# Optimization experiments

Hardware: AMD Instinct MI355X
Metric: run time of the kernel (lower is better)

## Reference

```python
import jax, jax.numpy as jnp
import numpy as np

N, CIN, COUT, E, NDIR = 65536, 128, 128, 589824, 9


def sel_conv(x, src, dst, sel, W, b):
    # x: [N, Cin]; W: [D, Cin, Cout]; edges j->i: out[i] += x[j] @ W[sel]
    n = x.shape[0]
    xs = x[src]  # [E, Cin] gather
    out = jnp.zeros((n, W.shape[2]), x.dtype)
    for d in range(W.shape[0]):  # fixed small direction count (9 or 1)
        m = (sel == d).astype(x.dtype)[:, None]
        agg = jax.ops.segment_sum(xs * m, dst, num_segments=n)  # [N, Cin]
        out = out + agg @ W[d]
    return out + b


def bn_eval(x, g, be, rm, rv, eps=1e-5):
    return (x - rm) * (g * jax.lax.rsqrt(rv + eps)) + be


def setup_inputs() -> dict:
    key = jax.random.key(0)
    ks = jax.random.split(key, 24)
    s = 0.05
    inp = {
        "x": jax.random.normal(ks[0], (N, CIN), jnp.float32),
        "edge_index": jax.random.randint(ks[1], (2, E), 0, N),
        "selections": jax.random.randint(ks[2], (E,), 0, NDIR),
        "W1": jax.random.normal(ks[3], (NDIR, CIN, COUT), jnp.float32) * s,
        "b1": jax.random.normal(ks[4], (COUT,), jnp.float32) * s,
        "g1": 1.0 + jax.random.normal(ks[5], (COUT,), jnp.float32) * s,
        "be1": jax.random.normal(ks[6], (COUT,), jnp.float32) * s,
        "rm1": jax.random.normal(ks[7], (COUT,), jnp.float32) * s,
        "rv1": 0.5 + jax.random.uniform(ks[8], (COUT,), jnp.float32),
        "W2": jax.random.normal(ks[9], (NDIR, COUT, COUT), jnp.float32) * s,
        "b2": jax.random.normal(ks[10], (COUT,), jnp.float32) * s,
        "g2": 1.0 + jax.random.normal(ks[11], (COUT,), jnp.float32) * s,
        "be2": jax.random.normal(ks[12], (COUT,), jnp.float32) * s,
        "rm2": jax.random.normal(ks[13], (COUT,), jnp.float32) * s,
        "rv2": 0.5 + jax.random.uniform(ks[14], (COUT,), jnp.float32),
        "W3": jax.random.normal(ks[15], (1, CIN, COUT), jnp.float32) * s,
        "b3": jax.random.normal(ks[16], (COUT,), jnp.float32) * s,
        "g3": 1.0 + jax.random.normal(ks[17], (COUT,), jnp.float32) * s,
        "be3": jax.random.normal(ks[18], (COUT,), jnp.float32) * s,
        "rm3": jax.random.normal(ks[19], (COUT,), jnp.float32) * s,
        "rv3": 0.5 + jax.random.uniform(ks[20], (COUT,), jnp.float32),
    }
    return inp


def reference(x, edge_index, selections, W1, b1, g1, be1, rm1, rv1,
              W2, b2, g2, be2, rm2, rv2, W3, b3, g3, be3, rm3, rv3):
    src, dst = edge_index[0], edge_index[1]
    # conv1: SelectionConv(3x3) + BN + ELU
    h = jax.nn.elu(bn_eval(sel_conv(x, src, dst, selections, W1, b1), g1, be1, rm1, rv1))
    # conv2: SelectionConv(3x3) + BN + ELU
    h = jax.nn.elu(bn_eval(sel_conv(h, src, dst, selections, W2, b2), g2, be2, rm2, rv2))
    # conv3: SelectionConv(1x1) shortcut (only selection-0 edges)
    sc = sel_conv(x, src, dst, selections, W3, b3)
    return jax.nn.elu(bn_eval(h + sc, g3, be3, rm3, rv3))
```

## Files before the change

kernel.cpp:

```cpp
#include <hip/hip_runtime.h>
#include <hip/hip_bf16.h>
#include <math.h>

#define N_NODES 65536
#define NDIR 9
#define NEDGE 589824
#define NBINS (N_NODES*NDIR)
#define TILE_M 32
#define SKEY_CAP 1024

typedef __attribute__((ext_vector_type(8))) short short8;
typedef __attribute__((ext_vector_type(4))) float f32x4;

__device__ inline float bf2f(unsigned short u){ return __uint_as_float(((unsigned int)u)<<16); }
__device__ inline unsigned short f2bf(float f){
  unsigned int x = __float_as_uint(f);
  x += 0x7fff + ((x>>16)&1);
  return (unsigned short)(x>>16);
}
__device__ inline float elu1(float x){ return x>0.f ? x : expm1f(x); }

__global__ void prep_w(const float* __restrict__ W1, const float* __restrict__ W2,
                       const float* __restrict__ W3,
                       const float* __restrict__ g1, const float* __restrict__ rv1,
                       const float* __restrict__ g2, const float* __restrict__ rv2,
                       const float* __restrict__ g3, const float* __restrict__ rv3,
                       unsigned short* __restrict__ Wt1, unsigned short* __restrict__ Wt2){
  int idx = blockIdx.x*256 + threadIdx.x;
  const float eps = 1e-5f;
  if (idx < 1280*128) {
    int n = idx >> 7, k = idx & 127;
    float v;
    if (n < 1152) { int d = n >> 7, c = n & 127;
      float s = g1[c]*rsqrtf(rv1[c]+eps); v = W1[(d*128 + k)*128 + c] * s; }
    else { int c = n - 1152;
      float s = g3[c]*rsqrtf(rv3[c]+eps); v = W3[k*128 + c] * s; }
    Wt1[idx] = f2bf(v);
  } else {
    int j = idx - 1280*128;
    int n = j >> 7, k = j & 127;
    int d = n >> 7, c = n & 127;
    float s = g2[c]*rsqrtf(rv2[c]+eps);
    Wt2[j] = f2bf(W2[(d*128 + k)*128 + c] * s);
  }
}

__global__ void prep_bias(const float* b1,const float* g1,const float* be1,const float* rm1,const float* rv1,
                          const float* b2,const float* g2,const float* be2,const float* rm2,const float* rv2,
                          const float* b3,const float* g3,const float* be3,const float* rm3,const float* rv3,
                          float* bias1, float* bias2, float* bias3, float* s3v){
  int c = threadIdx.x;
  const float eps = 1e-5f;
  float s1 = g1[c]*rsqrtf(rv1[c]+eps);
  bias1[c] = (b1[c]-rm1[c])*s1 + be1[c];
  float s2 = g2[c]*rsqrtf(rv2[c]+eps);
  bias2[c] = (b2[c]-rm2[c])*s2 + be2[c];
  float s3 = g3[c]*rsqrtf(rv3[c]+eps);
  bias3[c] = (b3[c]-rm3[c])*s3 + be3[c];
  s3v[c] = s3;
}

__global__ void xcast_k(const float* __restrict__ x, unsigned short* __restrict__ xb){
  int i = (blockIdx.x*256 + threadIdx.x)*8;
  f32x4 f0 = *(const f32x4*)(x + i);
  f32x4 f1 = *(const f32x4*)(x + i + 4);
  short8 t;
  #pragma unroll
  for (int j = 0; j < 4; j++){ t[j] = (short)f2bf(f0[j]); t[4+j] = (short)f2bf(f1[j]); }
  *(short8*)(xb + i) = t;
}

__global__ void hist_k(const int* __restrict__ dst, const int* __restrict__ sel,
                       int* __restrict__ hist){
  int e = blockIdx.x*256 + threadIdx.x;
  atomicAdd(&hist[dst[e]*9 + sel[e]], 1);
}

__global__ void scan1_k(const int* __restrict__ in, int* __restrict__ out, int* __restrict__ bsum){
  __shared__ int wsum[4];
  int t = threadIdx.x;
  int base = blockIdx.x*1024 + t*4;
  int4 v = *(const int4*)(in + base);
  int s = v.x + v.y + v.z + v.w;
  int lane = t & 63, w = t >> 6;
  int inc = s;
  #pragma unroll
  for (int o = 1; o < 64; o <<= 1){ int n = __shfl_up(inc, o); if (lane >= o) inc += n; }
  if (lane == 63) wsum[w] = inc;
  __syncthreads();
  int acc = 0;
  for (int i = 0; i < w; i++) acc += wsum[i];
  int ex = acc + inc - s;
  out[base] = ex; out[base+1] = ex + v.x; out[base+2] = ex + v.x + v.y; out[base+3] = ex + v.x + v.y + v.z;
  if (t == 255) bsum[blockIdx.x] = acc + inc;
}

__global__ void scan3_k(int* __restrict__ rs, const int* __restrict__ bsumx, int* __restrict__ cursor){
  int i = blockIdx.x*256 + threadIdx.x;
  int v = rs[i] + bsumx[i >> 10];
  rs[i] = v; cursor[i] = v;
  if (i == 0) rs[NBINS] = NEDGE;
}

__global__ void scatter_k(const int* __restrict__ src, const int* __restrict__ dst,
                          const int* __restrict__ sel,
                          int* __restrict__ cursor, int* __restrict__ sorted){
  int e = blockIdx.x*256 + threadIdx.x;
  int bin = dst[e]*9 + sel[e];
  int pos = atomicAdd(&cursor[bin], 1);
  sorted[pos] = src[e];
}

__device__ __forceinline__ void mfma_tile(f32x4 acc[2][2],
                                          const unsigned short* agg,
                                          const unsigned short* __restrict__ Wd,
                                          int w, int q, int r){
  #pragma unroll
  for (int kk = 0; kk < 4; kk++){
    const unsigned short* wp = Wd + (size_t)(w*32 + r)*128 + kk*32 + q*8;
    short8 b0 = *(const short8*)wp;
    short8 b1 = *(const short8*)(wp + 16*128);
    #pragma unroll
    for (int mt = 0; mt < 2; mt++){
      short8 av = *(const short8*)&agg[(mt*16 + r)*136 + kk*32 + q*8];
      acc[mt][0] = __builtin_amdgcn_mfma_f32_16x16x32_bf16(av, b0, acc[mt][0], 0, 0, 0);
      acc[mt][1] = __builtin_amdgcn_mfma_f32_16x16x32_bf16(av, b1, acc[mt][1], 0, 0, 0);
    }
  }
}

template<int IS_L2>
__global__ __launch_bounds__(256, 8) void layer_k(
    const unsigned short* __restrict__ H,
    const unsigned short* __restrict__ X,
    const unsigned short* __restrict__ Wf,
    const unsigned short* __restrict__ W3f,
    const int* __restrict__ rs, const int* __restrict__ sorted,
    const float* __restrict__ biasA, const float* __restrict__ bias3,
    const float* __restrict__ s3v,
    unsigned short* __restrict__ outB, float* __restrict__ outF){
  __shared__ __align__(16) unsigned short agg[TILE_M*136];
  __shared__ int skey[SKEY_CAP];
  __shared__ int rsl[TILE_M*9 + 1];
  const int tid = threadIdx.x;
  const int w = tid >> 6, lane = tid & 63;
  const int q = lane >> 4, r = lane & 15;
  const int rid = tid >> 4, c = tid & 15;
  const int m0 = blockIdx.x * TILE_M;

  for (int i = tid; i <= TILE_M*9; i += 256) rsl[i] = rs[m0*9 + i];
  __syncthreads();
  const int lo = rsl[0];
  const int cnt = rsl[TILE_M*9] - lo;
  for (int i = tid; i < cnt && i < SKEY_CAP; i += 256) skey[i] = sorted[lo + i];

  f32x4 acc[2][2];
  #pragma unroll
  for (int mt = 0; mt < 2; mt++){ acc[mt][0] = (f32x4){0,0,0,0}; acc[mt][1] = (f32x4){0,0,0,0}; }

  #pragma unroll 1
  for (int d = 0; d < 9; d++){
    __syncthreads();
    #pragma unroll
    for (int t = 0; t < 2; t++){
      int nl = t*16 + rid;
      int b = nl*9 + d;
      int s = rsl[b] - lo, e = rsl[b+1] - lo;
      f32x4 a0 = {0,0,0,0}, a1 = {0,0,0,0};
      for (int i = s; i < e; i++){
        int key = (i < SKEY_CAP) ? skey[i] : sorted[lo + i];
        short8 v = *(const short8*)(H + (size_t)key*128 + c*8);
        a0[0] += bf2f((unsigned short)v[0]); a0[1] += bf2f((unsigned short)v[1]);
        a0[2] += bf2f((unsigned short)v[2]); a0[3] += bf2f((unsigned short)v[3]);
        a1[0] += bf2f((unsigned short)v[4]); a1[1] += bf2f((unsigned short)v[5]);
        a1[2] += bf2f((unsigned short)v[6]); a1[3] += bf2f((unsigned short)v[7]);
      }
      short8 o;
      o[0]=(short)f2bf(a0[0]); o[1]=(short)f2bf(a0[1]); o[2]=(short)f2bf(a0[2]); o[3]=(short)f2bf(a0[3]);
      o[4]=(short)f2bf(a1[0]); o[5]=(short)f2bf(a1[1]); o[6]=(short)f2bf(a1[2]); o[7]=(short)f2bf(a1[3]);
      *(short8*)&agg[nl*136 + c*8] = o;
    }
    __syncthreads();
    mfma_tile(acc, agg, Wf + (size_t)d*128*128, w, q, r);
  }

  if constexpr (!IS_L2){
    #pragma unroll
    for (int mt = 0; mt < 2; mt++)
      #pragma unroll
      for (int n2 = 0; n2 < 2; n2++){
        int col = w*32 + n2*16 + r;
        float bA = biasA[col];
        #pragma unroll
        for (int rr = 0; rr < 4; rr++){
          int row = m0 + mt*16 + q*4 + rr;
          outB[(size_t)row*128 + col] = f2bf(elu1(acc[mt][n2][rr] + bA));
        }
      }
  } else {
    f32x4 sca[2][2];
    #pragma unroll
    for (int mt = 0; mt < 2; mt++){ sca[mt][0] = (f32x4){0,0,0,0}; sca[mt][1] = (f32x4){0,0,0,0}; }
    __syncthreads();
    #pragma unroll
    for (int t = 0; t < 2; t++){
      int nl = t*16 + rid;
      int b = nl*9;
      int s = rsl[b] - lo, e = rsl[b+1] - lo;
      f32x4 a0 = {0,0,0,0}, a1 = {0,0,0,0};
      for (int i = s; i < e; i++){
        int key = (i < SKEY_CAP) ? skey[i] : sorted[lo + i];
        short8 v = *(const short8*)(X + (size_t)key*128 + c*8);
        a0[0] += bf2f((unsigned short)v[0]); a0[1] += bf2f((unsigned short)v[1]);
        a0[2] += bf2f((unsigned short)v[2]); a0[3] += bf2f((unsigned short)v[3]);
        a1[0] += bf2f((unsigned short)v[4]); a1[1] += bf2f((unsigned short)v[5]);
        a1[2] += bf2f((unsigned short)v[6]); a1[3] += bf2f((unsigned short)v[7]);
      }
      short8 o;
      o[0]=(short)f2bf(a0[0]); o[1]=(short)f2bf(a0[1]); o[2]=(short)f2bf(a0[2]); o[3]=(short)f2bf(a0[3]);
      o[4]=(short)f2bf(a1[0]); o[5]=(short)f2bf(a1[1]); o[6]=(short)f2bf(a1[2]); o[7]=(short)f2bf(a1[3]);
      *(short8*)&agg[nl*136 + c*8] = o;
    }
    __syncthreads();
    mfma_tile(sca, agg, W3f, w, q, r);
    #pragma unroll
    for (int mt = 0; mt < 2; mt++)
      #pragma unroll
      for (int n2 = 0; n2 < 2; n2++){
        int col = w*32 + n2*16 + r;
        float bA = biasA[col], b3 = bias3[col], s3 = s3v[col];
        #pragma unroll
        for (int rr = 0; rr < 4; rr++){
          int row = m0 + mt*16 + q*4 + rr;
          float h = elu1(acc[mt][n2][rr] + bA);
          outF[(size_t)row*128 + col] = elu1(h*s3 + sca[mt][n2][rr] + b3);
        }
      }
  }
}

extern "C" void kernel_launch(void* const* d_in, const int* in_sizes, int n_in,
                              void* d_out, int out_size, void* d_ws, size_t ws_size,
                              hipStream_t stream){
  const float* x   = (const float*)d_in[0];
  const int*   ei  = (const int*)d_in[1];
  const int*   sel = (const int*)d_in[2];
  const float* W1  = (const float*)d_in[3];
  const float* b1  = (const float*)d_in[4];
  const float* g1  = (const float*)d_in[5];
  const float* be1 = (const float*)d_in[6];
  const float* rm1 = (const float*)d_in[7];
  const float* rv1 = (const float*)d_in[8];
  const float* W2  = (const float*)d_in[9];
  const float* b2  = (const float*)d_in[10];
  const float* g2  = (const float*)d_in[11];
  const float* be2 = (const float*)d_in[12];
  const float* rm2 = (const float*)d_in[13];
  const float* rv2 = (const float*)d_in[14];
  const float* W3  = (const float*)d_in[15];
  const float* b3  = (const float*)d_in[16];
  const float* g3  = (const float*)d_in[17];
  const float* be3 = (const float*)d_in[18];
  const float* rm3 = (const float*)d_in[19];
  const float* rv3 = (const float*)d_in[20];

  char* ws = (char*)d_ws;
  unsigned short* xb   = (unsigned short*)(ws);
  unsigned short* h1   = (unsigned short*)(ws + 16777216);
  unsigned short* Wt1  = (unsigned short*)(ws + 33554432);
  unsigned short* Wt2  = (unsigned short*)(ws + 33882112);
  float* bias1  = (float*)(ws + 34177024);
  float* bias2  = bias1 + 128;
  float* bias3  = bias1 + 256;
  float* s3v    = bias1 + 384;
  int* hist     = (int*)(ws + 34179072);
  int* rs       = (int*)(ws + 36538368);
  int* cursor   = (int*)(ws + 38897920);
  int* bsum     = (int*)(ws + 41257216);
  int* bsumx    = (int*)(ws + 41261312);
  int* bsumT    = (int*)(ws + 41265408);
  int* sorted   = (int*)(ws + 41265664);

  const int* srcp = ei;
  const int* dstp = ei + NEDGE;

  hipMemsetAsync(hist, 0, NBINS*sizeof(int), stream);
  prep_w<<<1216, 256, 0, stream>>>(W1, W2, W3, g1, rv1, g2, rv2, g3, rv3, Wt1, Wt2);
  prep_bias<<<1, 128, 0, stream>>>(b1,g1,be1,rm1,rv1, b2,g2,be2,rm2,rv2, b3,g3,be3,rm3,rv3,
                                   bias1, bias2, bias3, s3v);
  xcast_k<<<4096, 256, 0, stream>>>(x, xb);
  hist_k<<<NEDGE/256, 256, 0, stream>>>(dstp, sel, hist);
  scan1_k<<<NBINS/1024, 256, 0, stream>>>(hist, rs, bsum);
  scan1_k<<<1, 256, 0, stream>>>(bsum, bsumx, bsumT);
  scan3_k<<<NBINS/256, 256, 0, stream>>>(rs, bsumx, cursor);
  scatter_k<<<NEDGE/256, 256, 0, stream>>>(srcp, dstp, sel, cursor, sorted);

  layer_k<0><<<2048, 256, 0, stream>>>(xb, nullptr, Wt1, nullptr, rs, sorted,
                                       bias1, nullptr, nullptr, h1, nullptr);
  layer_k<1><<<2048, 256, 0, stream>>>(h1, xb, Wt2, Wt1 + 1152*128, rs, sorted,
                                       bias2, bias3, s3v, nullptr, (float*)d_out);
}
```

Measured before the change: 369.9 us.

## Fuse prep kernels into one launch and prefetch first gather row per bin

Merges the hist memset, weight prep, bias prep and x cast into a single prep_all kernel to cut launch count. In the layer kernel, each thread prefetches the first neighbor row of the next direction bin (and, in layer 2, of the shortcut bin) during the current iteration, so the gather latency overlaps with the MFMA phase. This costs extra registers and some speculative loads for empty bins, clamped to stay in bounds.

```diff
diff --git a/kernel.cpp b/kernel.cpp
--- a/kernel.cpp
+++ b/kernel.cpp
@@ -8,6 +8,7 @@
 #define NBINS (N_NODES*NDIR)
 #define TILE_M 32
 #define SKEY_CAP 1024
+#define APITCH 136
 
 typedef __attribute__((ext_vector_type(8))) short short8;
 typedef __attribute__((ext_vector_type(4))) float f32x4;
@@ -20,54 +21,71 @@
 }
 __device__ inline float elu1(float x){ return x>0.f ? x : expm1f(x); }
 
-__global__ void prep_w(const float* __restrict__ W1, const float* __restrict__ W2,
-                       const float* __restrict__ W3,
-                       const float* __restrict__ g1, const float* __restrict__ rv1,
-                       const float* __restrict__ g2, const float* __restrict__ rv2,
-                       const float* __restrict__ g3, const float* __restrict__ rv3,
-                       unsigned short* __restrict__ Wt1, unsigned short* __restrict__ Wt2){
-  int idx = blockIdx.x*256 + threadIdx.x;
+__device__ inline void acc8(f32x4& a0, f32x4& a1, short8 v){
+  a0[0] += bf2f((unsigned short)v[0]); a0[1] += bf2f((unsigned short)v[1]);
+  a0[2] += bf2f((unsigned short)v[2]); a0[3] += bf2f((unsigned short)v[3]);
+  a1[0] += bf2f((unsigned short)v[4]); a1[1] += bf2f((unsigned short)v[5]);
+  a1[2] += bf2f((unsigned short)v[6]); a1[3] += bf2f((unsigned short)v[7]);
+}
+
+__global__ void prep_all(const float* __restrict__ x, unsigned short* __restrict__ xb,
+                         const float* __restrict__ W1, const float* __restrict__ W2,
+                         const float* __restrict__ W3,
+                         const float* __restrict__ b1, const float* __restrict__ g1,
+                         const float* __restrict__ be1, const float* __restrict__ rm1,
+                         const float* __restrict__ rv1,
+                         const float* __restrict__ b2, const float* __restrict__ g2,
+                         const float* __restrict__ be2, const float* __restrict__ rm2,
+                         const float* __restrict__ rv2,
+                         const float* __restrict__ b3, const float* __restrict__ g3,
+                         const float* __restrict__ be3, const float* __restrict__ rm3,
+                         const float* __restrict__ rv3,
+                         unsigned short* __restrict__ Wt1, unsigned short* __restrict__ Wt2,
+                         float* __restrict__ bias1, float* __restrict__ bias2,
+                         float* __restrict__ bias3, float* __restrict__ s3v,
+                         int* __restrict__ hist){
   const float eps = 1e-5f;
-  if (idx < 1280*128) {
-    int n = idx >> 7, k = idx & 127;
-    float v;
-    if (n < 1152) { int d = n >> 7, c = n & 127;
-      float s = g1[c]*rsqrtf(rv1[c]+eps); v = W1[(d*128 + k)*128 + c] * s; }
-    else { int c = n - 1152;
-      float s = g3[c]*rsqrtf(rv3[c]+eps); v = W3[k*128 + c] * s; }
-    Wt1[idx] = f2bf(v);
+  int b = blockIdx.x, tid = threadIdx.x;
+  if (b < 576){
+    int4 z = {0,0,0,0};
+    *(int4*)&hist[(b*256 + tid)*4] = z;
+  } else if (b < 1792){
+    int idx = (b - 576)*256 + tid;
+    if (idx < 1280*128) {
+      int n = idx >> 7, k = idx & 127;
+      float v;
+      if (n < 1152) { int d = n >> 7, c = n & 127;
+        float s = g1[c]*rsqrtf(rv1[c]+eps); v = W1[(d*128 + k)*128 + c] * s; }
+      else { int c = n - 1152;
+        float s = g3[c]*rsqrtf(rv3[c]+eps); v = W3[k*128 + c] * s; }
+      Wt1[idx] = f2bf(v);
+    } else {
+      int j = idx - 1280*128;
+      int n = j >> 7, k = j & 127;
+      int d = n >> 7, c = n & 127;
+      float s = g2[c]*rsqrtf(rv2[c]+eps);
+      Wt2[j] = f2bf(W2[(d*128 + k)*128 + c] * s);
+    }
+  } else if (b == 1792){
+    if (tid < 128){
+      int c = tid;
+      float s1 = g1[c]*rsqrtf(rv1[c]+eps);
+      bias1[c] = (b1[c]-rm1[c])*s1 + be1[c];
+      float s2 = g2[c]*rsqrtf(rv2[c]+eps);
+      bias2[c] = (b2[c]-rm2[c])*s2 + be2[c];
+      float s3 = g3[c]*rsqrtf(rv3[c]+eps);
+      bias3[c] = (b3[c]-rm3[c])*s3 + be3[c];
+      s3v[c] = s3;
+    }
   } else {
-    int j = idx - 1280*128;
-    int n = j >> 7, k = j & 127;
-    int d = n >> 7, c = n & 127;
-    float s = g2[c]*rsqrtf(rv2[c]+eps);
-    Wt2[j] = f2bf(W2[(d*128 + k)*128 + c] * s);
-  }
-}
-
-__global__ void prep_bias(const float* b1,const float* g1,const float* be1,const float* rm1,const float* rv1,
-                          const float* b2,const float* g2,const float* be2,const float* rm2,const float* rv2,
-                          const float* b3,const float* g3,const float* be3,const float* rm3,const float* rv3,
-                          float* bias1, float* bias2, float* bias3, float* s3v){
-  int c = threadIdx.x;
-  const float eps = 1e-5f;
-  float s1 = g1[c]*rsqrtf(rv1[c]+eps);
-  bias1[c] = (b1[c]-rm1[c])*s1 + be1[c];
-  float s2 = g2[c]*rsqrtf(rv2[c]+eps);
-  bias2[c] = (b2[c]-rm2[c])*s2 + be2[c];
-  float s3 = g3[c]*rsqrtf(rv3[c]+eps);
-  bias3[c] = (b3[c]-rm3[c])*s3 + be3[c];
-  s3v[c] = s3;
-}
-
-__global__ void xcast_k(const float* __restrict__ x, unsigned short* __restrict__ xb){
-  int i = (blockIdx.x*256 + threadIdx.x)*8;
-  f32x4 f0 = *(const f32x4*)(x + i);
-  f32x4 f1 = *(const f32x4*)(x + i + 4);
-  short8 t;
-  #pragma unroll
-  for (int j = 0; j < 4; j++){ t[j] = (short)f2bf(f0[j]); t[4+j] = (short)f2bf(f1[j]); }
-  *(short8*)(xb + i) = t;
+    int i = ((b - 1793)*256 + tid)*8;
+    f32x4 f0 = *(const f32x4*)(x + i);
+    f32x4 f1 = *(const f32x4*)(x + i + 4);
+    short8 t;
+    #pragma unroll
+    for (int j = 0; j < 4; j++){ t[j] = (short)f2bf(f0[j]); t[4+j] = (short)f2bf(f1[j]); }
+    *(short8*)(xb + i) = t;
+  }
 }
 
 __global__ void hist_k(const int* __restrict__ dst, const int* __restrict__ sel,
@@ -122,7 +140,7 @@
     short8 b1 = *(const short8*)(wp + 16*128);
     #pragma unroll
     for (int mt = 0; mt < 2; mt++){
-      short8 av = *(const short8*)&agg[(mt*16 + r)*136 + kk*32 + q*8];
+      short8 av = *(const short8*)&agg[(mt*16 + r)*APITCH + kk*32 + q*8];
       acc[mt][0] = __builtin_amdgcn_mfma_f32_16x16x32_bf16(av, b0, acc[mt][0], 0, 0, 0);
       acc[mt][1] = __builtin_amdgcn_mfma_f32_16x16x32_bf16(av, b1, acc[mt][1], 0, 0, 0);
     }
@@ -139,7 +157,7 @@
     const float* __restrict__ biasA, const float* __restrict__ bias3,
     const float* __restrict__ s3v,
     unsigned short* __restrict__ outB, float* __restrict__ outF){
-  __shared__ __align__(16) unsigned short agg[TILE_M*136];
+  __shared__ __align__(16) unsigned short agg[TILE_M*APITCH];
   __shared__ int skey[SKEY_CAP];
   __shared__ int rsl[TILE_M*9 + 1];
   const int tid = threadIdx.x;
@@ -152,6 +170,17 @@
   __syncthreads();
   const int lo = rsl[0];
   const int cnt = rsl[TILE_M*9] - lo;
+
+  short8 pvA, pvB;
+  {
+    int aA = rsl[rid*9];
+    int aB = rsl[(16+rid)*9];
+    if (aA > NEDGE-1) aA = NEDGE-1;
+    if (aB > NEDGE-1) aB = NEDGE-1;
+    pvA = *(const short8*)(H + (size_t)sorted[aA]*128 + c*8);
+    pvB = *(const short8*)(H + (size_t)sorted[aB]*128 + c*8);
+  }
+
   for (int i = tid; i < cnt && i < SKEY_CAP; i += 256) skey[i] = sorted[lo + i];
 
   f32x4 acc[2][2];
@@ -161,24 +190,54 @@
   #pragma unroll 1
   for (int d = 0; d < 9; d++){
     __syncthreads();
-    #pragma unroll
-    for (int t = 0; t < 2; t++){
-      int nl = t*16 + rid;
-      int b = nl*9 + d;
+    {
+      int b = rid*9 + d;
       int s = rsl[b] - lo, e = rsl[b+1] - lo;
       f32x4 a0 = {0,0,0,0}, a1 = {0,0,0,0};
-      for (int i = s; i < e; i++){
-        int key = (i < SKEY_CAP) ? skey[i] : sorted[lo + i];
-        short8 v = *(const short8*)(H + (size_t)key*128 + c*8);
-        a0[0] += bf2f((unsigned short)v[0]); a0[1] += bf2f((unsigned short)v[1]);
-        a0[2] += bf2f((unsigned short)v[2]); a0[3] += bf2f((unsigned short)v[3]);
-        a1[0] += bf2f((unsigned short)v[4]); a1[1] += bf2f((unsigned short)v[5]);
-        a1[2] += bf2f((unsigned short)v[6]); a1[3] += bf2f((unsigned short)v[7]);
+      if (e > s){
+        acc8(a0, a1, pvA);
+        for (int i = s+1; i < e; i++){
+          int key = (i < SKEY_CAP) ? skey[i] : sorted[lo + i];
+          short8 v = *(const short8*)(H + (size_t)key*128 + c*8);
+          acc8(a0, a1, v);
+        }
       }
       short8 o;
       o[0]=(short)f2bf(a0[0]); o[1]=(short)f2bf(a0[1]); o[2]=(short)f2bf(a0[2]); o[3]=(short)f2bf(a0[3]);
       o[4]=(short)f2bf(a1[0]); o[5]=(short)f2bf(a1[1]); o[6]=(short)f2bf(a1[2]); o[7]=(short)f2bf(a1[3]);
-      *(short8*)&agg[nl*136 + c*8] = o;
+      *(short8*)&agg[rid*APITCH + c*8] = o;
+    }
+    {
+      int b = (16 + rid)*9 + d;
+      int s = rsl[b] - lo, e = rsl[b+1] - lo;
+      f32x4 a0 = {0,0,0,0}, a1 = {0,0,0,0};
+      if (e > s){
+        acc8(a0, a1, pvB);
+        for (int i = s+1; i < e; i++){
+          int key = (i < SKEY_CAP) ? skey[i] : sorted[lo + i];
+          short8 v = *(const short8*)(H + (size_t)key*128 + c*8);
+          acc8(a0, a1, v);
+        }
+      }
+      short8 o;
+      o[0]=(short)f2bf(a0[0]); o[1]=(short)f2bf(a0[1]); o[2]=(short)f2bf(a0[2]); o[3]=(short)f2bf(a0[3]);
+      o[4]=(short)f2bf(a1[0]); o[5]=(short)f2bf(a1[1]); o[6]=(short)f2bf(a1[2]); o[7]=(short)f2bf(a1[3]);
+      *(short8*)&agg[(16 + rid)*APITCH + c*8] = o;
+    }
+    if (d < 8){
+      int aA = rsl[rid*9 + d + 1];
+      int aB = rsl[(16+rid)*9 + d + 1];
+      if (aA > NEDGE-1) aA = NEDGE-1;
+      if (aB > NEDGE-1) aB = NEDGE-1;
+      pvA = *(const short8*)(H + (size_t)sorted[aA]*128 + c*8);
+      pvB = *(const short8*)(H + (size_t)sorted[aB]*128 + c*8);
+    } else if (IS_L2){
+      int aA = rsl[rid*9];
+      int aB = rsl[(16+rid)*9];
+      if (aA > NEDGE-1) aA = NEDGE-1;
+      if (aB > NEDGE-1) aB = NEDGE-1;
+      pvA = *(const short8*)(X + (size_t)sorted[aA]*128 + c*8);
+      pvB = *(const short8*)(X + (size_t)sorted[aB]*128 + c*8);
     }
     __syncthreads();
     mfma_tile(acc, agg, Wf + (size_t)d*128*128, w, q, r);
@@ -198,30 +257,45 @@
         }
       }
   } else {
-    f32x4 sca[2][2];
-    #pragma unroll
-    for (int mt = 0; mt < 2; mt++){ sca[mt][0] = (f32x4){0,0,0,0}; sca[mt][1] = (f32x4){0,0,0,0}; }
     __syncthreads();
-    #pragma unroll
-    for (int t = 0; t < 2; t++){
-      int nl = t*16 + rid;
-      int b = nl*9;
+    {
+      int b = rid*9;
       int s = rsl[b] - lo, e = rsl[b+1] - lo;
       f32x4 a0 = {0,0,0,0}, a1 = {0,0,0,0};
-      for (int i = s; i < e; i++){
-        int key = (i < SKEY_CAP) ? skey[i] : sorted[lo + i];
-        short8 v = *(const short8*)(X + (size_t)key*128 + c*8);
-        a0[0] += bf2f((unsigned short)v[0]); a0[1] += bf2f((unsigned short)v[1]);
-        a0[2] += bf2f((unsigned short)v[2]); a0[3] += bf2f((unsigned short)v[3]);
-        a1[0] += bf2f((unsigned short)v[4]); a1[1] += bf2f((unsigned short)v[5]);
-        a1[2] += bf2f((unsigned short)v[6]); a1[3] += bf2f((unsigned short)v[7]);
+      if (e > s){
+        acc8(a0, a1, pvA);
+        for (int i = s+1; i < e; i++){
+          int key = (i < SKEY_CAP) ? skey[i] : sorted[lo + i];
+          short8 v = *(const short8*)(X + (size_t)key*128 + c*8);
+          acc8(a0, a1, v);
+        }
       }
       short8 o;
       o[0]=(short)f2bf(a0[0]); o[1]=(short)f2bf(a0[1]); o[2]=(short)f2bf(a0[2]); o[3]=(short)f2bf(a0[3]);
       o[4]=(short)f2bf(a1[0]); o[5]=(short)f2bf(a1[1]); o[6]=(short)f2bf(a1[2]); o[7]=(short)f2bf(a1[3]);
-      *(short8*)&agg[nl*136 + c*8] = o;
+      *(short8*)&agg[rid*APITCH + c*8] = o;
+    }
+    {
+      int b = (16 + rid)*9;
+      int s = rsl[b] - lo, e = rsl[b+1] - lo;
+      f32x4 a0 = {0,0,0,0}, a1 = {0,0,0,0};
+      if (e > s){
+        acc8(a0, a1, pvB);
+        for (int i = s+1; i < e; i++){
+          int key = (i < SKEY_CAP) ? skey[i] : sorted[lo + i];
+          short8 v = *(const short8*)(X + (size_t)key*128 + c*8);
+          acc8(a0, a1, v);
+        }
+      }
+      short8 o;
+      o[0]=(short)f2bf(a0[0]); o[1]=(short)f2bf(a0[1]); o[2]=(short)f2bf(a0[2]); o[3]=(short)f2bf(a0[3]);
+      o[4]=(short)f2bf(a1[0]); o[5]=(short)f2bf(a1[1]); o[6]=(short)f2bf(a1[2]); o[7]=(short)f2bf(a1[3]);
+      *(short8*)&agg[(16 + rid)*APITCH + c*8] = o;
     }
     __syncthreads();
+    f32x4 sca[2][2];
+    #pragma unroll
+    for (int mt = 0; mt < 2; mt++){ sca[mt][0] = (f32x4){0,0,0,0}; sca[mt][1] = (f32x4){0,0,0,0}; }
     mfma_tile(sca, agg, W3f, w, q, r);
     #pragma unroll
     for (int mt = 0; mt < 2; mt++)
@@ -284,11 +358,11 @@
   const int* srcp = ei;
   const int* dstp = ei + NEDGE;
 
-  hipMemsetAsync(hist, 0, NBINS*sizeof(int), stream);
-  prep_w<<<1216, 256, 0, stream>>>(W1, W2, W3, g1, rv1, g2, rv2, g3, rv3, Wt1, Wt2);
-  prep_bias<<<1, 128, 0, stream>>>(b1,g1,be1,rm1,rv1, b2,g2,be2,rm2,rv2, b3,g3,be3,rm3,rv3,
-                                   bias1, bias2, bias3, s3v);
-  xcast_k<<<4096, 256, 0, stream>>>(x, xb);
+  prep_all<<<5889, 256, 0, stream>>>(x, xb, W1, W2, W3,
+                                     b1, g1, be1, rm1, rv1,
+                                     b2, g2, be2, rm2, rv2,
+                                     b3, g3, be3, rm3, rv3,
+                                     Wt1, Wt2, bias1, bias2, bias3, s3v, hist);
   hist_k<<<NEDGE/256, 256, 0, stream>>>(dstp, sel, hist);
   scan1_k<<<NBINS/1024, 256, 0, stream>>>(hist, rs, bsum);
   scan1_k<<<1, 256, 0, stream>>>(bsum, bsumx, bsumT);
```

Result: no change. 371.4 us (+0.4%).
